# Kernel tuning notes

Hardware: AMD Instinct MI355X
Metric: run time of the kernel (lower is better)

Reference implementation:

```python
import jax, jax.numpy as jnp
import numpy as np

N_NODES = 100000
N_EDGES = 20000
NNZ = 800000
D_IN = 256
D_OUT = 256


def _segment_mean(feats, seg_ids, num_segments):
    # feats: [nnz, d] gathered features; seg_ids: [nnz] target segment per entry
    s = jax.ops.segment_sum(feats, seg_ids, num_segments=num_segments)
    cnt = jax.ops.segment_sum(jnp.ones((seg_ids.shape[0],), feats.dtype), seg_ids,
                              num_segments=num_segments)
    return s / jnp.maximum(cnt, 1.0)[:, None]


def setup_inputs() -> dict:
    key = jax.random.key(0)
    k1, k2, k3, k4, k5 = jax.random.split(key, 5)
    X = jax.random.normal(k1, (N_NODES, D_IN), dtype=jnp.float32)
    W = jax.random.normal(k2, (D_IN, D_OUT), dtype=jnp.float32) * (1.0 / np.sqrt(D_IN))
    b = jax.random.normal(k3, (D_OUT,), dtype=jnp.float32) * 0.01
    vertex_idx = jax.random.randint(k4, (NNZ,), 0, N_NODES, dtype=jnp.int32)
    edge_idx = jax.random.randint(k5, (NNZ,), 0, N_EDGES, dtype=jnp.int32)
    return {"X": X, "W": W, "b": b, "vertex_idx": vertex_idx, "edge_idx": edge_idx}


def reference(X, W, b, vertex_idx, edge_idx):
    # theta: linear projection
    H = X @ W + b                                   # [N_NODES, D_OUT]
    # v2e mean: hyperedge feature = mean of incident vertex features
    Y = _segment_mean(H[vertex_idx], edge_idx, N_EDGES)   # [N_EDGES, D_OUT]
    # e2v mean: vertex feature = mean of incident hyperedge features
    X_ = _segment_mean(Y[edge_idx], vertex_idx, N_NODES)  # [N_NODES, D_OUT]
    # ReLU; dropout is identity in eval mode
    return jax.nn.relu(X_)
```

## Files before the change

### kernel.cpp

```cpp
#include <hip/hip_runtime.h>
#include <hip/hip_bf16.h>

constexpr int N_NODES = 100000;
constexpr int N_EDGES = 20000;
constexpr int NNZ     = 800000;
constexpr int D       = 256;

typedef unsigned short ushort_t;
typedef unsigned short ushort4v __attribute__((ext_vector_type(4)));
typedef unsigned short ushort8v __attribute__((ext_vector_type(8)));
typedef __bf16         bf16x8   __attribute__((ext_vector_type(8)));
typedef float          f32x4    __attribute__((ext_vector_type(4)));
typedef float          f32x8    __attribute__((ext_vector_type(8)));
typedef unsigned long long u64;
typedef unsigned long long u64x2 __attribute__((ext_vector_type(2)));

static __device__ inline ushort_t f2bf(float f) {
  unsigned u = __builtin_bit_cast(unsigned, f);
  return (ushort_t)((u + 0x7FFFu + ((u >> 16) & 1u)) >> 16);
}

static __device__ inline f32x8 row_f32(const ushort_t* p) {
  bf16x8 b = __builtin_bit_cast(bf16x8, *(const ushort8v*)p);
  return __builtin_convertvector(b, f32x8);
}

static __device__ inline int bsum(u64 x) {
  return (int)((x * 0x0101010101010101ULL) >> 56);
}

constexpr int HCHUNKS   = 32;
constexpr int CHUNK4    = NNZ / 4 / HCHUNKS;
constexpr int PWORDS    = HCHUNKS / 8;
constexpr int NH_RANGES = 5;
constexpr int NH_BINS   = N_NODES / NH_RANGES;
constexpr int NH_BLOCKS = NH_RANGES * HCHUNKS;
constexpr int EH_BLOCKS = HCHUNKS;
constexpr int HIST_BLOCKS  = NH_BLOCKS + EH_BLOCKS;
constexpr int TRANS_BLOCKS = 64;
constexpr int CAST_BLOCKS  = 6250;
constexpr int PREP_BLOCKS  = HIST_BLOCKS + TRANS_BLOCKS + CAST_BLOCKS;
constexpr int HWORDS = 5000;

__global__ __launch_bounds__(256) void prep_kernel(
    const float* __restrict__ X, const float* __restrict__ W,
    const int* __restrict__ vidx, const int* __restrict__ eidx,
    ushort_t* __restrict__ Xb, ushort_t* __restrict__ Wt,
    unsigned char* __restrict__ pe, unsigned char* __restrict__ pn,
    unsigned char* __restrict__ lre, unsigned char* __restrict__ lrn) {
  __shared__ unsigned int hist[HWORDS];
  const int blk = blockIdx.x, tid = threadIdx.x;
  if (blk < HIST_BLOCKS) {
    const bool is_n = blk < NH_BLOCKS;
    const int c  = is_n ? (blk & (HCHUNKS - 1)) : (blk - NH_BLOCKS);
    const int lo = is_n ? (blk >> 5) * NH_BINS : 0;
    const int* __restrict__ idx = is_n ? vidx : eidx;
    unsigned char* __restrict__ lr = is_n ? lrn : lre;
    for (int t = tid; t < HWORDS; t += 256) hist[t] = 0;
    __syncthreads();
    const int base4 = c * CHUNK4;
    for (int k = tid; k < CHUNK4; k += 256) {
      int i4 = base4 + k;
      int4 q = ((const int4*)idx)[i4];
      int vv[4] = {q.x, q.y, q.z, q.w};
#pragma unroll
      for (int j = 0; j < 4; ++j) {
        unsigned rel = (unsigned)(vv[j] - lo);
        if (rel < (unsigned)NH_BINS) {
          unsigned sh = 8u * (rel & 3u);
          unsigned old = atomicAdd(&hist[rel >> 2], 1u << sh);
          lr[(size_t)i4 * 4 + j] = (unsigned char)((old >> sh) & 0xFFu);
        }
      }
    }
    __syncthreads();
    unsigned char* __restrict__ pb = is_n ? pn : pe;
    for (int t = tid; t < NH_BINS; t += 256) {
      unsigned byte = (hist[t >> 2] >> (8u * (t & 3u))) & 0xFFu;
      pb[(size_t)(lo + t) * HCHUNKS + c] = (unsigned char)byte;
    }
  } else if (blk < HIST_BLOCKS + TRANS_BLOCKS) {
    int wb = blk - HIST_BLOCKS;
#pragma unroll
    for (int i = 0; i < 4; ++i) {
      int k = wb * 4 + i;
      Wt[(size_t)tid * 256 + k] = f2bf(W[(size_t)k * 256 + tid]);
    }
  } else {
    int cb = blk - HIST_BLOCKS - TRANS_BLOCKS;
#pragma unroll
    for (int q = 0; q < 4; ++q) {
      int idx4 = cb * 1024 + q * 256 + tid;
      float4 v = ((const float4*)X)[idx4];
      ushort4v o = { f2bf(v.x), f2bf(v.y), f2bf(v.z), f2bf(v.w) };
      *(ushort4v*)&Xb[(size_t)idx4 * 4] = o;
    }
  }
}

constexpr int SCAN_L    = N_EDGES + N_NODES;
constexpr int SCAN_TPB  = 1024;
constexpr int SCAN_EPT  = 4;
constexpr int SCAN_TILE = SCAN_TPB * SCAN_EPT;
constexpr int SCAN_NB   = (SCAN_L + SCAN_TILE - 1) / SCAN_TILE;

static __device__ inline int bsum32(const u64* P) {
  u64x2 a = *(const u64x2*)P;
  u64x2 b = *(const u64x2*)(P + 2);
  return bsum(a[0]) + bsum(a[1]) + bsum(b[0]) + bsum(b[1]);
}

__global__ __launch_bounds__(1024) void scan_phaseA(
    const u64* __restrict__ pe, const u64* __restrict__ pn,
    int* __restrict__ comb, int* __restrict__ btot) {
  __shared__ int wsum[16];
  const int tid = threadIdx.x, lane = tid & 63, wid = tid >> 6;
  const int base = blockIdx.x * SCAN_TILE + tid * SCAN_EPT;
  int v[SCAN_EPT];
#pragma unroll
  for (int i = 0; i < SCAN_EPT; ++i) {
    int j = base + i;
    int x = 0;
    if (j < SCAN_L)
      x = bsum32(j < N_EDGES ? pe + (size_t)j * PWORDS
                             : pn + (size_t)(j - N_EDGES) * PWORDS);
    v[i] = x;
  }
  int tsum = v[0] + v[1] + v[2] + v[3];
  int x = tsum;
#pragma unroll
  for (int d = 1; d < 64; d <<= 1) {
    int y = __shfl_up(x, (unsigned)d, 64);
    if (lane >= d) x += y;
  }
  if (lane == 63) wsum[wid] = x;
  __syncthreads();
  if (wid == 0) {
    int s = (lane < 16) ? wsum[lane] : 0;
#pragma unroll
    for (int d = 1; d < 16; d <<= 1) {
      int y = __shfl_up(s, (unsigned)d, 64);
      if (lane >= d) s += y;
    }
    if (lane < 16) wsum[lane] = s;
  }
  __syncthreads();
  int texcl = ((wid == 0) ? 0 : wsum[wid - 1]) + (x - tsum);
  int run = texcl;
#pragma unroll
  for (int i = 0; i < SCAN_EPT; ++i) {
    int j = base + i;
    if (j < SCAN_L) comb[j] = run;
    run += v[i];
  }
  if (tid == 0) btot[blockIdx.x] = wsum[15];
}

__global__ __launch_bounds__(1024) void scan_phaseC(
    const int* __restrict__ comb, const int* __restrict__ btot,
    int* __restrict__ eoff, int* __restrict__ noff) {
  int add = 0;
  for (int bdx = 0; bdx < blockIdx.x; ++bdx) add += btot[bdx];
  const int base = blockIdx.x * SCAN_TILE + threadIdx.x * SCAN_EPT;
#pragma unroll
  for (int i = 0; i < SCAN_EPT; ++i) {
    int j = base + i;
    if (j < SCAN_L) {
      int val = comb[j] + add;
      if (j < N_EDGES) eoff[j] = val;
      else             noff[j - N_EDGES] = val - NNZ;
    }
  }
  if (blockIdx.x == 0 && threadIdx.x == 0) {
    eoff[N_EDGES] = NNZ;
    noff[N_NODES] = NNZ;
  }
}

__global__ __launch_bounds__(256) void scatter_calc(
    const int* __restrict__ vidx, const int* __restrict__ eidx,
    const int* __restrict__ eoff, const int* __restrict__ noff,
    const u64* __restrict__ pe, const u64* __restrict__ pn,
    const unsigned char* __restrict__ lre, const unsigned char* __restrict__ lrn,
    int* __restrict__ evals, int* __restrict__ nvals) {
  int i4 = blockIdx.x * 256 + threadIdx.x;
  if (i4 >= NNZ / 4) return;
  int c = i4 / CHUNK4;
  int w = c >> 3, sub = c & 7;
  u64 mw = (1ULL << (8 * sub)) - 1ULL;
  u64 m0 = (w > 0) ? ~0ULL : mw;
  u64 m1 = (w > 1) ? ~0ULL : ((w == 1) ? mw : 0ULL);
  u64 m2 = (w > 2) ? ~0ULL : ((w == 2) ? mw : 0ULL);
  u64 m3 = (w == 3) ? mw : 0ULL;
  int4 e4 = ((const int4*)eidx)[i4];
  int4 v4 = ((const int4*)vidx)[i4];
  unsigned le = *(const unsigned*)(lre + (size_t)i4 * 4);
  unsigned ln = *(const unsigned*)(lrn + (size_t)i4 * 4);
  int ee[4] = {e4.x, e4.y, e4.z, e4.w};
  int vv[4] = {v4.x, v4.y, v4.z, v4.w};
#pragma unroll
  for (int j = 0; j < 4; ++j) {
    int e = ee[j], v = vv[j];
    u64x2 ea = *(const u64x2*)(pe + (size_t)e * PWORDS);
    u64x2 eb = *(const u64x2*)(pe + (size_t)e * PWORDS + 2);
    u64x2 na = *(const u64x2*)(pn + (size_t)v * PWORDS);
    u64x2 nb = *(const u64x2*)(pn + (size_t)v * PWORDS + 2);
    int pre_e = bsum(ea[0] & m0) + bsum(ea[1] & m1) + bsum(eb[0] & m2) + bsum(eb[1] & m3);
    int pre_n = bsum(na[0] & m0) + bsum(na[1] & m1) + bsum(nb[0] & m2) + bsum(nb[1] & m3);
    int re = (int)((le >> (8 * j)) & 0xFFu);
    int rn = (int)((ln >> (8 * j)) & 0xFFu);
    evals[eoff[e] + pre_e + re] = v;
    nvals[noff[v] + pre_n + rn] = e;
  }
}

constexpr int V2E_NBLK = N_EDGES / 4;
__global__ __launch_bounds__(256) void v2e_mean_q(
    const ushort_t* __restrict__ Xb, const int* __restrict__ eoff,
    const int* __restrict__ evals, ushort_t* __restrict__ Xeb) {
  int q    = blockIdx.x / V2E_NBLK;
  int blk  = blockIdx.x - q * V2E_NBLK;
  int wave = threadIdx.x >> 6, lane = threadIdx.x & 63;
  int g = lane >> 3, l8 = lane & 7;
  int seg = blk * 4 + wave;
  int s = eoff[seg], e = eoff[seg + 1];
  const ushort_t* base = Xb + q * 64 + l8 * 8;
  f32x8 acc = {0, 0, 0, 0, 0, 0, 0, 0};
#pragma unroll 2
  for (int j = s + g; j < e; j += 8)
    acc += row_f32(&base[(size_t)evals[j] * 256]);
#pragma unroll
  for (int i = 0; i < 8; ++i) {
    acc[i] += __shfl_xor(acc[i], 8, 64);
    acc[i] += __shfl_xor(acc[i], 16, 64);
    acc[i] += __shfl_xor(acc[i], 32, 64);
  }
  if (g == 0) {
    float inv = 1.0f / (float)max(e - s, 1);
    ushort8v o;
#pragma unroll
    for (int i = 0; i < 8; ++i) o[i] = f2bf(acc[i] * inv);
    *(ushort8v*)&Xeb[(size_t)seg * 256 + q * 64 + l8 * 8] = o;
  }
}

__global__ __launch_bounds__(256) void gemm_mfma(
    const ushort_t* __restrict__ A, const ushort_t* __restrict__ Wt,
    const float* __restrict__ bias, ushort_t* __restrict__ Ye) {
  const int w = threadIdx.x >> 6, lane = threadIdx.x & 63;
  const int m15 = lane & 15, q = lane >> 4;
  const int m0 = blockIdx.x * 16;
  const ushort_t* arow = A + (size_t)(m0 + m15) * 256 + q * 8;
  f32x4 acc[4] = { {0,0,0,0}, {0,0,0,0}, {0,0,0,0}, {0,0,0,0} };
  for (int k0 = 0; k0 < 256; k0 += 32) {
    bf16x8 af = __builtin_bit_cast(bf16x8, *(const ushort8v*)(arow + k0));
#pragma unroll
    for (int t = 0; t < 4; ++t) {
      const ushort_t* brow = Wt + (size_t)(w * 64 + t * 16 + m15) * 256 + k0 + q * 8;
      bf16x8 bf = __builtin_bit_cast(bf16x8, *(const ushort8v*)brow);
      acc[t] = __builtin_amdgcn_mfma_f32_16x16x32_bf16(af, bf, acc[t], 0, 0, 0);
    }
  }
#pragma unroll
  for (int t = 0; t < 4; ++t) {
    int col = w * 64 + t * 16 + m15;
    float bv = bias[col];
#pragma unroll
    for (int r = 0; r < 4; ++r) {
      int row = m0 + q * 4 + r;
      Ye[(size_t)row * 256 + col] = f2bf(acc[t][r] + bv);
    }
  }
}

constexpr int E2V_NBLK = N_NODES / 4;
__global__ __launch_bounds__(256) void e2v_mean_relu_q(
    const ushort_t* __restrict__ Yeb, const int* __restrict__ noff,
    const int* __restrict__ nvals, float* __restrict__ dst) {
  int q    = blockIdx.x / E2V_NBLK;
  int blk  = blockIdx.x - q * E2V_NBLK;
  int wave = threadIdx.x >> 6, lane = threadIdx.x & 63;
  int g = lane >> 3, l8 = lane & 7;
  int seg = blk * 4 + wave;
  int s = noff[seg], e = noff[seg + 1];
  const ushort_t* base = Yeb + q * 64 + l8 * 8;
  f32x8 acc = {0, 0, 0, 0, 0, 0, 0, 0};
#pragma unroll 2
  for (int j = s + g; j < e; j += 8)
    acc += row_f32(&base[(size_t)nvals[j] * 256]);
#pragma unroll
  for (int i = 0; i < 8; ++i) {
    acc[i] += __shfl_xor(acc[i], 8, 64);
    acc[i] += __shfl_xor(acc[i], 16, 64);
    acc[i] += __shfl_xor(acc[i], 32, 64);
  }
  if (g == 0) {
    float inv = 1.0f / (float)max(e - s, 1);
    float4 o0, o1;
    o0.x = fmaxf(acc[0] * inv, 0.f); o0.y = fmaxf(acc[1] * inv, 0.f);
    o0.z = fmaxf(acc[2] * inv, 0.f); o0.w = fmaxf(acc[3] * inv, 0.f);
    o1.x = fmaxf(acc[4] * inv, 0.f); o1.y = fmaxf(acc[5] * inv, 0.f);
    o1.z = fmaxf(acc[6] * inv, 0.f); o1.w = fmaxf(acc[7] * inv, 0.f);
    size_t b = (size_t)seg * 256 + q * 64 + l8 * 8;
    *(float4*)&dst[b]     = o0;
    *(float4*)&dst[b + 4] = o1;
  }
}

constexpr size_t OFF_XB    = 0;
constexpr size_t OFF_XEB   = OFF_XB  + (size_t)N_NODES * D * 2;
constexpr size_t OFF_YEB   = OFF_XEB + (size_t)N_EDGES * D * 2;
constexpr size_t OFF_WT    = OFF_YEB + (size_t)N_EDGES * D * 2;
constexpr size_t OFF_PE    = OFF_WT  + (size_t)D * D * 2;
constexpr size_t OFF_PN    = OFF_PE  + (size_t)N_EDGES * HCHUNKS;
constexpr size_t OFF_LRE   = OFF_PN  + (size_t)N_NODES * HCHUNKS;
constexpr size_t OFF_LRN   = OFF_LRE + (size_t)NNZ;
constexpr size_t OFF_EOFF  = OFF_LRN + (size_t)NNZ;
constexpr size_t OFF_NOFF  = OFF_EOFF + (size_t)(N_EDGES + 1 + 3) * 4;
constexpr size_t OFF_EVALS = OFF_NOFF + (size_t)(N_NODES + 1 + 3) * 4;
constexpr size_t OFF_NVALS = OFF_EVALS + (size_t)NNZ * 4;
constexpr size_t OFF_COMB  = OFF_NVALS + (size_t)NNZ * 4;
constexpr size_t OFF_BTOT  = OFF_COMB + (size_t)SCAN_L * 4;

extern "C" void kernel_launch(void* const* d_in, const int* in_sizes, int n_in,
                              void* d_out, int out_size, void* d_ws, size_t ws_size,
                              hipStream_t stream) {
  const float* X    = (const float*)d_in[0];
  const float* W    = (const float*)d_in[1];
  const float* b    = (const float*)d_in[2];
  const int*   vidx = (const int*)d_in[3];
  const int*   eidx = (const int*)d_in[4];
  float*       out  = (float*)d_out;

  char* ws = (char*)d_ws;
  ushort_t* Xb   = (ushort_t*)(ws + OFF_XB);
  ushort_t* Xeb  = (ushort_t*)(ws + OFF_XEB);
  ushort_t* Yeb  = (ushort_t*)(ws + OFF_YEB);
  ushort_t* Wt   = (ushort_t*)(ws + OFF_WT);
  unsigned char* pe_b = (unsigned char*)(ws + OFF_PE);
  unsigned char* pn_b = (unsigned char*)(ws + OFF_PN);
  u64* pe_u = (u64*)(ws + OFF_PE);
  u64* pn_u = (u64*)(ws + OFF_PN);
  unsigned char* lre = (unsigned char*)(ws + OFF_LRE);
  unsigned char* lrn = (unsigned char*)(ws + OFF_LRN);
  int* eoff  = (int*)(ws + OFF_EOFF);
  int* noff  = (int*)(ws + OFF_NOFF);
  int* evals = (int*)(ws + OFF_EVALS);
  int* nvals = (int*)(ws + OFF_NVALS);
  int* comb  = (int*)(ws + OFF_COMB);
  int* btot  = (int*)(ws + OFF_BTOT);


  prep_kernel<<<PREP_BLOCKS, 256, 0, stream>>>(X, W, vidx, eidx, Xb, Wt,
                                               pe_b, pn_b, lre, lrn);

  scan_phaseA<<<SCAN_NB, SCAN_TPB, 0, stream>>>(pe_u, pn_u, comb, btot);
  scan_phaseC<<<SCAN_NB, SCAN_TPB, 0, stream>>>(comb, btot, eoff, noff);

  scatter_calc<<<(NNZ / 4 + 255) / 256, 256, 0, stream>>>(
      vidx, eidx, eoff, noff, pe_u, pn_u, lre, lrn, evals, nvals);

  v2e_mean_q<<<4 * V2E_NBLK, 256, 0, stream>>>(Xb, eoff, evals, Xeb);

  gemm_mfma<<<N_EDGES / 16, 256, 0, stream>>>(Xeb, Wt, b, Yeb);

  e2v_mean_relu_q<<<4 * E2V_NBLK, 256, 0, stream>>>(Yeb, noff, nvals, out);
}
```

Baseline: 445.1 us.

## Gather fp32 X directly in v2e, drop bf16 cast pass, restructure segment mappings

Removes the full X-to-bf16 cast pass in the prep kernel. The v2e mean now gathers fp32 rows of X directly, with one wave per segment, 4 floats per lane and 4 independent accumulators. The e2v mean now maps a half-wave to each node and reads whole bf16 rows, instead of splitting columns into quarters across separate blocks. This avoids writing and re-reading a 51 MB bf16 copy, at the cost of gathering twice the bytes per row in v2e and serial per-wave loops over segments.

```diff
diff --git a/kernel.cpp b/kernel.cpp
--- a/kernel.cpp
+++ b/kernel.cpp
@@ -38,14 +38,13 @@
 constexpr int EH_BLOCKS = HCHUNKS;
 constexpr int HIST_BLOCKS  = NH_BLOCKS + EH_BLOCKS;
 constexpr int TRANS_BLOCKS = 64;
-constexpr int CAST_BLOCKS  = 6250;
-constexpr int PREP_BLOCKS  = HIST_BLOCKS + TRANS_BLOCKS + CAST_BLOCKS;
+constexpr int PREP_BLOCKS  = HIST_BLOCKS + TRANS_BLOCKS;
 constexpr int HWORDS = 5000;
 
 __global__ __launch_bounds__(256) void prep_kernel(
-    const float* __restrict__ X, const float* __restrict__ W,
+    const float* __restrict__ W,
     const int* __restrict__ vidx, const int* __restrict__ eidx,
-    ushort_t* __restrict__ Xb, ushort_t* __restrict__ Wt,
+    ushort_t* __restrict__ Wt,
     unsigned char* __restrict__ pe, unsigned char* __restrict__ pn,
     unsigned char* __restrict__ lre, unsigned char* __restrict__ lrn) {
   __shared__ unsigned int hist[HWORDS];
@@ -79,21 +78,12 @@
       unsigned byte = (hist[t >> 2] >> (8u * (t & 3u))) & 0xFFu;
       pb[(size_t)(lo + t) * HCHUNKS + c] = (unsigned char)byte;
     }
-  } else if (blk < HIST_BLOCKS + TRANS_BLOCKS) {
+  } else {
     int wb = blk - HIST_BLOCKS;
 #pragma unroll
     for (int i = 0; i < 4; ++i) {
       int k = wb * 4 + i;
       Wt[(size_t)tid * 256 + k] = f2bf(W[(size_t)k * 256 + tid]);
-    }
-  } else {
-    int cb = blk - HIST_BLOCKS - TRANS_BLOCKS;
-#pragma unroll
-    for (int q = 0; q < 4; ++q) {
-      int idx4 = cb * 1024 + q * 256 + tid;
-      float4 v = ((const float4*)X)[idx4];
-      ushort4v o = { f2bf(v.x), f2bf(v.y), f2bf(v.z), f2bf(v.w) };
-      *(ushort4v*)&Xb[(size_t)idx4 * 4] = o;
     }
   }
 }
@@ -214,34 +204,30 @@
   }
 }
 
-constexpr int V2E_NBLK = N_EDGES / 4;
-__global__ __launch_bounds__(256) void v2e_mean_q(
-    const ushort_t* __restrict__ Xb, const int* __restrict__ eoff,
+__global__ __launch_bounds__(256) void v2e_mean_f32(
+    const float* __restrict__ X, const int* __restrict__ eoff,
     const int* __restrict__ evals, ushort_t* __restrict__ Xeb) {
-  int q    = blockIdx.x / V2E_NBLK;
-  int blk  = blockIdx.x - q * V2E_NBLK;
   int wave = threadIdx.x >> 6, lane = threadIdx.x & 63;
-  int g = lane >> 3, l8 = lane & 7;
-  int seg = blk * 4 + wave;
+  int seg = blockIdx.x * 4 + wave;
   int s = eoff[seg], e = eoff[seg + 1];
-  const ushort_t* base = Xb + q * 64 + l8 * 8;
-  f32x8 acc = {0, 0, 0, 0, 0, 0, 0, 0};
-#pragma unroll 2
-  for (int j = s + g; j < e; j += 8)
-    acc += row_f32(&base[(size_t)evals[j] * 256]);
-#pragma unroll
-  for (int i = 0; i < 8; ++i) {
-    acc[i] += __shfl_xor(acc[i], 8, 64);
-    acc[i] += __shfl_xor(acc[i], 16, 64);
-    acc[i] += __shfl_xor(acc[i], 32, 64);
-  }
-  if (g == 0) {
-    float inv = 1.0f / (float)max(e - s, 1);
-    ushort8v o;
-#pragma unroll
-    for (int i = 0; i < 8; ++i) o[i] = f2bf(acc[i] * inv);
-    *(ushort8v*)&Xeb[(size_t)seg * 256 + q * 64 + l8 * 8] = o;
-  }
+  const float* base = X + lane * 4;
+  f32x4 a0 = {0, 0, 0, 0}, a1 = a0, a2 = a0, a3 = a0;
+  int j = s;
+  for (; j + 3 < e; j += 4) {
+    int r0 = evals[j], r1 = evals[j + 1], r2 = evals[j + 2], r3 = evals[j + 3];
+    a0 += *(const f32x4*)&base[(size_t)r0 * 256];
+    a1 += *(const f32x4*)&base[(size_t)r1 * 256];
+    a2 += *(const f32x4*)&base[(size_t)r2 * 256];
+    a3 += *(const f32x4*)&base[(size_t)r3 * 256];
+  }
+  for (; j < e; ++j)
+    a0 += *(const f32x4*)&base[(size_t)evals[j] * 256];
+  a0 = (a0 + a1) + (a2 + a3);
+  float inv = 1.0f / (float)max(e - s, 1);
+  ushort4v o;
+#pragma unroll
+  for (int i = 0; i < 4; ++i) o[i] = f2bf(a0[i] * inv);
+  *(ushort4v*)&Xeb[(size_t)seg * 256 + lane * 4] = o;
 }
 
 __global__ __launch_bounds__(256) void gemm_mfma(
@@ -273,42 +259,34 @@
   }
 }
 
-constexpr int E2V_NBLK = N_NODES / 4;
-__global__ __launch_bounds__(256) void e2v_mean_relu_q(
+__global__ __launch_bounds__(256) void e2v_mean_relu(
     const ushort_t* __restrict__ Yeb, const int* __restrict__ noff,
     const int* __restrict__ nvals, float* __restrict__ dst) {
-  int q    = blockIdx.x / E2V_NBLK;
-  int blk  = blockIdx.x - q * E2V_NBLK;
-  int wave = threadIdx.x >> 6, lane = threadIdx.x & 63;
-  int g = lane >> 3, l8 = lane & 7;
-  int seg = blk * 4 + wave;
+  int half = threadIdx.x >> 5, l32 = threadIdx.x & 31;
+  int seg = blockIdx.x * 8 + half;
   int s = noff[seg], e = noff[seg + 1];
-  const ushort_t* base = Yeb + q * 64 + l8 * 8;
-  f32x8 acc = {0, 0, 0, 0, 0, 0, 0, 0};
-#pragma unroll 2
-  for (int j = s + g; j < e; j += 8)
-    acc += row_f32(&base[(size_t)nvals[j] * 256]);
-#pragma unroll
-  for (int i = 0; i < 8; ++i) {
-    acc[i] += __shfl_xor(acc[i], 8, 64);
-    acc[i] += __shfl_xor(acc[i], 16, 64);
-    acc[i] += __shfl_xor(acc[i], 32, 64);
-  }
-  if (g == 0) {
-    float inv = 1.0f / (float)max(e - s, 1);
-    float4 o0, o1;
-    o0.x = fmaxf(acc[0] * inv, 0.f); o0.y = fmaxf(acc[1] * inv, 0.f);
-    o0.z = fmaxf(acc[2] * inv, 0.f); o0.w = fmaxf(acc[3] * inv, 0.f);
-    o1.x = fmaxf(acc[4] * inv, 0.f); o1.y = fmaxf(acc[5] * inv, 0.f);
-    o1.z = fmaxf(acc[6] * inv, 0.f); o1.w = fmaxf(acc[7] * inv, 0.f);
-    size_t b = (size_t)seg * 256 + q * 64 + l8 * 8;
-    *(float4*)&dst[b]     = o0;
-    *(float4*)&dst[b + 4] = o1;
-  }
-}
-
-constexpr size_t OFF_XB    = 0;
-constexpr size_t OFF_XEB   = OFF_XB  + (size_t)N_NODES * D * 2;
+  const ushort_t* base = Yeb + l32 * 8;
+  f32x8 a0 = {0, 0, 0, 0, 0, 0, 0, 0}, a1 = a0;
+  int j = s;
+  for (; j + 1 < e; j += 2) {
+    int r0 = nvals[j], r1 = nvals[j + 1];
+    a0 += row_f32(&base[(size_t)r0 * 256]);
+    a1 += row_f32(&base[(size_t)r1 * 256]);
+  }
+  if (j < e) a0 += row_f32(&base[(size_t)nvals[j] * 256]);
+  a0 += a1;
+  float inv = 1.0f / (float)max(e - s, 1);
+  float4 o0, o1;
+  o0.x = fmaxf(a0[0] * inv, 0.f); o0.y = fmaxf(a0[1] * inv, 0.f);
+  o0.z = fmaxf(a0[2] * inv, 0.f); o0.w = fmaxf(a0[3] * inv, 0.f);
+  o1.x = fmaxf(a0[4] * inv, 0.f); o1.y = fmaxf(a0[5] * inv, 0.f);
+  o1.z = fmaxf(a0[6] * inv, 0.f); o1.w = fmaxf(a0[7] * inv, 0.f);
+  size_t b = (size_t)seg * 256 + l32 * 8;
+  *(float4*)&dst[b]     = o0;
+  *(float4*)&dst[b + 4] = o1;
+}
+
+constexpr size_t OFF_XEB   = 0;
 constexpr size_t OFF_YEB   = OFF_XEB + (size_t)N_EDGES * D * 2;
 constexpr size_t OFF_WT    = OFF_YEB + (size_t)N_EDGES * D * 2;
 constexpr size_t OFF_PE    = OFF_WT  + (size_t)D * D * 2;
@@ -333,7 +311,6 @@
   float*       out  = (float*)d_out;
 
   char* ws = (char*)d_ws;
-  ushort_t* Xb   = (ushort_t*)(ws + OFF_XB);
   ushort_t* Xeb  = (ushort_t*)(ws + OFF_XEB);
   ushort_t* Yeb  = (ushort_t*)(ws + OFF_YEB);
   ushort_t* Wt   = (ushort_t*)(ws + OFF_WT);
@@ -351,7 +328,7 @@
   int* btot  = (int*)(ws + OFF_BTOT);
 
 
-  prep_kernel<<<PREP_BLOCKS, 256, 0, stream>>>(X, W, vidx, eidx, Xb, Wt,
+  prep_kernel<<<PREP_BLOCKS, 256, 0, stream>>>(W, vidx, eidx, Wt,
                                                pe_b, pn_b, lre, lrn);
 
   scan_phaseA<<<SCAN_NB, SCAN_TPB, 0, stream>>>(pe_u, pn_u, comb, btot);
@@ -360,9 +337,9 @@
   scatter_calc<<<(NNZ / 4 + 255) / 256, 256, 0, stream>>>(
       vidx, eidx, eoff, noff, pe_u, pn_u, lre, lrn, evals, nvals);
 
-  v2e_mean_q<<<4 * V2E_NBLK, 256, 0, stream>>>(Xb, eoff, evals, Xeb);
+  v2e_mean_f32<<<N_EDGES / 4, 256, 0, stream>>>(X, eoff, evals, Xeb);
 
   gemm_mfma<<<N_EDGES / 16, 256, 0, stream>>>(Xeb, Wt, b, Yeb);
 
-  e2v_mean_relu_q<<<4 * E2V_NBLK, 256, 0, stream>>>(Yeb, noff, nvals, out);
-}
+  e2v_mean_relu<<<N_NODES / 8, 256, 0, stream>>>(Yeb, noff, nvals, out);
+}
```

After: 421.9 us. 5.2% less time.
